# Performance work log

Hardware: AMD Instinct MI355X
Metric: run time of the kernel (lower is better)

## Reference

```python
import jax, jax.numpy as jnp
import numpy as np
import math

B = 8192
N_MODELS = 64
T_PER_SPLIT = 16
MAXLEAF = 64
EMB = 32
BN_EPS = 1e-5


def setup_inputs() -> dict:
    key = jax.random.key(0)
    k1, k2, k3 = jax.random.split(key, 3)
    # leaf indices per (sample, model*tree), values in [0, maxleaf)
    x = jax.random.randint(k1, (B, N_MODELS * T_PER_SPLIT), 0, MAXLEAF, dtype=jnp.int32)
    # embed_w ~ N(0, sqrt(1/max_ntree_per_split))
    embed_w = jax.random.normal(k2, (N_MODELS, T_PER_SPLIT * MAXLEAF, EMB), dtype=jnp.float32) * math.sqrt(1.0 / T_PER_SPLIT)
    # BatchNorm1d affine params (gamma=1, beta=0 at init)
    bn_gamma = jnp.ones((N_MODELS * EMB,), dtype=jnp.float32)
    bn_beta = jnp.zeros((N_MODELS * EMB,), dtype=jnp.float32)
    # BatchDense(n_models, embsize, 1): weight (M, E, 1) squeezed to (M, E), bias zeros (M,)
    stdv = math.sqrt(6.0 / (EMB + 1))
    bout_w = jax.random.uniform(k3, (N_MODELS, EMB), dtype=jnp.float32, minval=-stdv, maxval=stdv)
    bout_b = jnp.zeros((N_MODELS,), dtype=jnp.float32)
    return {"x": x, "embed_w": embed_w, "bn_gamma": bn_gamma, "bn_beta": bn_beta,
            "bout_w": bout_w, "bout_b": bout_b}


def reference(x, embed_w, bn_gamma, bn_beta, bout_w, bout_b):
    # x: (B, M*T) int leaf indices; embed_w: (M, T*L, E)
    Bn = x.shape[0]
    M, TL, E = embed_w.shape
    T = x.shape[1] // M
    L = TL // T
    # one_hot + bmm == per-tree gather from embed_w, summed over trees
    idx = x.reshape(Bn, M, T) + jnp.arange(T, dtype=x.dtype) * L  # (B, M, T) into TL axis
    emb = embed_w[jnp.arange(M)[None, :, None], idx]              # (B, M, T, E) gather
    h = emb.sum(axis=2).reshape(Bn, M * E)                        # (B, M*E)
    # BatchNorm1d (training-mode batch statistics, biased variance as in torch)
    mean = h.mean(axis=0)
    var = h.var(axis=0)
    h = (h - mean) / jnp.sqrt(var + BN_EPS) * bn_gamma + bn_beta
    # dropout is identity in eval mode
    h = h.reshape(Bn, M, E)
    # BatchDense: per-model linear E -> 1
    out = jnp.einsum('bme,me->bm', h, bout_w) + bout_b            # (B, M)
    sum_out = out.sum(axis=-1, keepdims=True)                     # (B, 1)
    return (sum_out, out)
```

## Files before the change

kernel.cpp:

```cpp
#include <hip/hip_runtime.h>
#include <hip/hip_fp16.h>

constexpr int B_TOT = 8192;
constexpr int NM    = 64;
constexpr int TT    = 16;
constexpr int LF    = 64;
constexpr int EM    = 32;
constexpr int XROW  = NM * TT;
constexpr int TROWS = TT * LF;

template<int TQ>
__device__ __forceinline__ int4 qbcast(int4 v) {
    constexpr int c = TQ * 0x55;
    int4 r;
    r.x = __builtin_amdgcn_mov_dpp(v.x, c, 0xf, 0xf, true);
    r.y = __builtin_amdgcn_mov_dpp(v.y, c, 0xf, 0xf, true);
    r.z = __builtin_amdgcn_mov_dpp(v.z, c, 0xf, 0xf, true);
    r.w = __builtin_amdgcn_mov_dpp(v.w, c, 0xf, 0xf, true);
    return r;
}

__device__ __forceinline__ __half2 H2(unsigned u) { return *(const __half2*)&u; }

__global__ __launch_bounds__(512, 4) void k_stats_f16(
    const int* __restrict__ x, const float* __restrict__ tbl,
    float* __restrict__ psum, float* __restrict__ psq)
{
    __shared__ uint4 tb[TROWS * 4];
    __shared__ float red[2][8][32];

    const int m     = blockIdx.x & 63;
    const int chunk = blockIdx.x >> 6;
    const int tid   = threadIdx.x;
    const int f     = tid & 3;
    const int grp   = tid >> 2;
    const int b0    = chunk * 1024;

    {
        const float4* __restrict__ src = (const float4*)(tbl + (size_t)m * (TROWS * EM));
#pragma unroll
        for (int i = 0; i < 8; ++i) {
            const int o = tid + i * 512;
            const float4 a = src[o * 2];
            const float4 c = src[o * 2 + 1];
            uint4 p;
            __half2 h0 = __floats2half2_rn(a.x, a.y);
            __half2 h1 = __floats2half2_rn(a.z, a.w);
            __half2 h2 = __floats2half2_rn(c.x, c.y);
            __half2 h3 = __floats2half2_rn(c.z, c.w);
            p.x = *(unsigned*)&h0; p.y = *(unsigned*)&h1;
            p.z = *(unsigned*)&h2; p.w = *(unsigned*)&h3;
            tb[o] = p;
        }
    }

    int4 xr = ((const int4*)(x + (size_t)(b0 + grp) * XROW + m * TT))[f];

    float s[8], s2[8];
#pragma unroll
    for (int k = 0; k < 8; ++k) { s[k] = 0.f; s2[k] = 0.f; }

    __syncthreads();

    for (int p = 0; p < 8; ++p) {
        int4 nxt;
        if (p < 7)
            nxt = ((const int4*)(x + (size_t)(b0 + (p + 1) * 128 + grp) * XROW + m * TT))[f];

        const int4 q0 = qbcast<0>(xr);
        const int4 q1 = qbcast<1>(xr);
        const int4 q2 = qbcast<2>(xr);
        const int4 q3 = qbcast<3>(xr);

        __half2 h0 = __half2(__half(0.f), __half(0.f));
        __half2 h1 = h0, h2 = h0, h3 = h0;

#define GATH(Q, RB)                                                          \
        {                                                                    \
            const uint4 a0 = tb[((Q).x + RB      ) * 4 + f];                 \
            const uint4 a1 = tb[((Q).y + RB +  64) * 4 + f];                 \
            const uint4 a2 = tb[((Q).z + RB + 128) * 4 + f];                 \
            const uint4 a3 = tb[((Q).w + RB + 192) * 4 + f];                 \
            h0 = __hadd2(h0, __hadd2(__hadd2(H2(a0.x), H2(a1.x)),            \
                                     __hadd2(H2(a2.x), H2(a3.x))));          \
            h1 = __hadd2(h1, __hadd2(__hadd2(H2(a0.y), H2(a1.y)),            \
                                     __hadd2(H2(a2.y), H2(a3.y))));          \
            h2 = __hadd2(h2, __hadd2(__hadd2(H2(a0.z), H2(a1.z)),            \
                                     __hadd2(H2(a2.z), H2(a3.z))));          \
            h3 = __hadd2(h3, __hadd2(__hadd2(H2(a0.w), H2(a1.w)),            \
                                     __hadd2(H2(a2.w), H2(a3.w))));          \
        }
        GATH(q0, 0) GATH(q1, 256) GATH(q2, 512) GATH(q3, 768)
#undef GATH

        const __half2 hv[4] = {h0, h1, h2, h3};
#pragma unroll
        for (int k = 0; k < 4; ++k) {
            const float lo = __low2float(hv[k]);
            const float hi = __high2float(hv[k]);
            s[2*k]   += lo;  s2[2*k]   = fmaf(lo, lo, s2[2*k]);
            s[2*k+1] += hi;  s2[2*k+1] = fmaf(hi, hi, s2[2*k+1]);
        }
        xr = nxt;
    }

#pragma unroll
    for (int off = 4; off <= 32; off <<= 1) {
#pragma unroll
        for (int k = 0; k < 8; ++k) {
            s[k]  += __shfl_xor(s[k],  off);
            s2[k] += __shfl_xor(s2[k], off);
        }
    }
    const int wave = tid >> 6;
    if ((tid & 63) < 4) {
#pragma unroll
        for (int k = 0; k < 8; ++k) {
            red[0][wave][f * 8 + k] = s[k];
            red[1][wave][f * 8 + k] = s2[k];
        }
    }
    __syncthreads();
    if (tid < 32) {
        float a = 0.f, a2 = 0.f;
#pragma unroll
        for (int w = 0; w < 8; ++w) { a += red[0][w][tid]; a2 += red[1][w][tid]; }
        psum[(chunk * NM + m) * EM + tid] = a;
        psq [(chunk * NM + m) * EM + tid] = a2;
    }
}

__global__ __launch_bounds__(256) void k_prep(
    const float* __restrict__ tbl,
    const float* __restrict__ gamma, const float* __restrict__ beta,
    const float* __restrict__ bw, const float* __restrict__ bb,
    const float* __restrict__ psum, const float* __restrict__ psq,
    float* __restrict__ Cm, float* __restrict__ g2)
{
    const int m    = blockIdx.x >> 2;
    const int part = blockIdx.x & 3;
    __shared__ float a_s[EM];
    if (threadIdx.x < EM) {
        const int e  = threadIdx.x;
        const int ch = m * EM + e;
        float sum = 0.f, sq = 0.f;
#pragma unroll
        for (int c = 0; c < 8; ++c) {
            sum += psum[(c * NM + m) * EM + e];
            sq  += psq [(c * NM + m) * EM + e];
        }
        const float inv_n = 1.f / (float)B_TOT;
        const float mean = sum * inv_n;
        const float var  = sq * inv_n - mean * mean;
        const float istd = rsqrtf(var + 1e-5f);
        const float g = gamma[ch];
        const float w = bw[ch];
        a_s[e] = istd * g * w;
        float ct = (beta[ch] - mean * istd * g) * w;
#pragma unroll
        for (int off = 16; off > 0; off >>= 1) ct += __shfl_down(ct, off, 32);
        if (e == 0 && part == 0) Cm[m] = bb[m] + ct;
    }
    __syncthreads();

    const float* __restrict__ tblm = tbl + (size_t)m * (TROWS * EM);
    const int row = part * 256 + threadIdx.x;
    const float4* rp = (const float4*)(tblm + row * EM);
    float acc = 0.f;
#pragma unroll
    for (int i = 0; i < 8; ++i) {
        const float4 v = rp[i];
        acc += v.x * a_s[i*4+0] + v.y * a_s[i*4+1]
             + v.z * a_s[i*4+2] + v.w * a_s[i*4+3];
    }
    g2[row * NM + m] = acc;
}

__global__ __launch_bounds__(1024, 8) void k_out(
    const int* __restrict__ x, const float* __restrict__ g2,
    const float* __restrict__ Cm, float* __restrict__ out)
{
    __shared__ float slab[4 * LF * NM];
    const int tid  = threadIdx.x;
    const int wid  = tid >> 6;
    const int lane = tid & 63;
    const int b    = blockIdx.x * 16 + wid;

    const int4* xp = (const int4*)(x + (size_t)b * XROW + lane * TT);
    const int4 q0 = xp[0], q1 = xp[1], q2 = xp[2], q3 = xp[3];
    const int idxs[16] = {q0.x,q0.y,q0.z,q0.w, q1.x,q1.y,q1.z,q1.w,
                          q2.x,q2.y,q2.z,q2.w, q3.x,q3.y,q3.z,q3.w};

    float acc = 0.f;
#pragma unroll
    for (int ph = 0; ph < 4; ++ph) {
        if (ph) __syncthreads();
        const float4* src = (const float4*)(g2 + (size_t)ph * (4 * LF * NM));
        float4* dst = (float4*)slab;
#pragma unroll
        for (int j = 0; j < 4; ++j) dst[tid + j * 1024] = src[tid + j * 1024];
        __syncthreads();
#pragma unroll
        for (int tt = 0; tt < 4; ++tt)
            acc += slab[tt * (LF * NM) + idxs[ph * 4 + tt] * NM + lane];
    }

    const float o = acc + Cm[lane];
    float s = o;
#pragma unroll
    for (int off = 32; off > 0; off >>= 1) s += __shfl_down(s, off);
    out[B_TOT + (size_t)b * NM + lane] = o;
    if (lane == 0) out[b] = s;
}

extern "C" void kernel_launch(void* const* d_in, const int* in_sizes, int n_in,
                              void* d_out, int out_size, void* d_ws, size_t ws_size,
                              hipStream_t stream) {
    const int*   x       = (const int*)d_in[0];
    const float* embed_w = (const float*)d_in[1];
    const float* gamma   = (const float*)d_in[2];
    const float* beta    = (const float*)d_in[3];
    const float* bout_w  = (const float*)d_in[4];
    const float* bout_b  = (const float*)d_in[5];
    float* out = (float*)d_out;

    float* ws   = (float*)d_ws;
    float* Cm   = ws;
    float* g2   = ws + 64;
    float* psum = ws + 64 + 65536;
    float* psq  = psum + 16384;

    k_stats_f16<<<dim3(512), dim3(512), 0, stream>>>(x, embed_w, psum, psq);
    k_prep<<<dim3(256), dim3(256),  0, stream>>>(embed_w, gamma, beta, bout_w,
                                                 bout_b, psum, psq, Cm, g2);
    k_out <<<dim3(512), dim3(1024), 0, stream>>>(x, g2, Cm, out);
}
```

Baseline: 108.0 us.

## Pack leaf indices to bytes in stats pass and process two samples per wave in output kernel

The stats kernel now writes a byte-packed copy of the leaf indices (four indices per 32-bit word) to workspace while it streams x. The output kernel reads this compact array, a quarter the size of the int32 x, instead of re-reading x. Each wave also handles two samples, so the g2 slab staged in shared memory is reused twice and only half the blocks are launched. The cost is an extra global write in the stats kernel, and the output kernel now depends on indices fitting in 8 bits.

Result: slower. 110.7 us (+2.5%).

```diff
diff --git a/kernel.cpp b/kernel.cpp
--- a/kernel.cpp
+++ b/kernel.cpp
@@ -24,7 +24,8 @@
 
 __global__ __launch_bounds__(512, 4) void k_stats_f16(
     const int* __restrict__ x, const float* __restrict__ tbl,
-    float* __restrict__ psum, float* __restrict__ psq)
+    float* __restrict__ psum, float* __restrict__ psq,
+    unsigned* __restrict__ x8)
 {
     __shared__ uint4 tb[TROWS * 4];
     __shared__ float red[2][8][32];
@@ -63,9 +64,14 @@
     __syncthreads();
 
     for (int p = 0; p < 8; ++p) {
+        const int b = b0 + p * 128 + grp;
         int4 nxt;
         if (p < 7)
-            nxt = ((const int4*)(x + (size_t)(b0 + (p + 1) * 128 + grp) * XROW + m * TT))[f];
+            nxt = ((const int4*)(x + (size_t)(b + 128) * XROW + m * TT))[f];
+
+        x8[((size_t)b * NM + m) * 4 + f] =
+            (unsigned)(xr.x & 0xff) | ((unsigned)(xr.y & 0xff) << 8) |
+            ((unsigned)(xr.z & 0xff) << 16) | ((unsigned)xr.w << 24);
 
         const int4 q0 = qbcast<0>(xr);
         const int4 q1 = qbcast<1>(xr);
@@ -176,22 +182,21 @@
     g2[row * NM + m] = acc;
 }
 
-__global__ __launch_bounds__(1024, 8) void k_out(
-    const int* __restrict__ x, const float* __restrict__ g2,
+__global__ __launch_bounds__(1024) void k_out(
+    const uint4* __restrict__ x8, const float* __restrict__ g2,
     const float* __restrict__ Cm, float* __restrict__ out)
 {
     __shared__ float slab[4 * LF * NM];
     const int tid  = threadIdx.x;
     const int wid  = tid >> 6;
     const int lane = tid & 63;
-    const int b    = blockIdx.x * 16 + wid;
-
-    const int4* xp = (const int4*)(x + (size_t)b * XROW + lane * TT);
-    const int4 q0 = xp[0], q1 = xp[1], q2 = xp[2], q3 = xp[3];
-    const int idxs[16] = {q0.x,q0.y,q0.z,q0.w, q1.x,q1.y,q1.z,q1.w,
-                          q2.x,q2.y,q2.z,q2.w, q3.x,q3.y,q3.z,q3.w};
-
-    float acc = 0.f;
+    const int bA   = blockIdx.x * 32 + wid;
+    const int bB   = bA + 16;
+
+    const uint4 pa = x8[(size_t)bA * NM + lane];
+    const uint4 pb = x8[(size_t)bB * NM + lane];
+
+    float accA = 0.f, accB = 0.f;
 #pragma unroll
     for (int ph = 0; ph < 4; ++ph) {
         if (ph) __syncthreads();
@@ -200,17 +205,30 @@
 #pragma unroll
         for (int j = 0; j < 4; ++j) dst[tid + j * 1024] = src[tid + j * 1024];
         __syncthreads();
-#pragma unroll
-        for (int tt = 0; tt < 4; ++tt)
-            acc += slab[tt * (LF * NM) + idxs[ph * 4 + tt] * NM + lane];
-    }
-
-    const float o = acc + Cm[lane];
-    float s = o;
-#pragma unroll
-    for (int off = 32; off > 0; off >>= 1) s += __shfl_down(s, off);
-    out[B_TOT + (size_t)b * NM + lane] = o;
-    if (lane == 0) out[b] = s;
+
+        const unsigned wa = (ph == 0) ? pa.x : (ph == 1) ? pa.y : (ph == 2) ? pa.z : pa.w;
+        const unsigned wb = (ph == 0) ? pb.x : (ph == 1) ? pb.y : (ph == 2) ? pb.z : pb.w;
+#pragma unroll
+        for (int k = 0; k < 4; ++k) {
+            const int ia = (wa >> (k * 8)) & 0xff;
+            const int ib = (wb >> (k * 8)) & 0xff;
+            accA += slab[k * (LF * NM) + ia * NM + lane];
+            accB += slab[k * (LF * NM) + ib * NM + lane];
+        }
+    }
+
+    const float cm = Cm[lane];
+    const float oA = accA + cm;
+    const float oB = accB + cm;
+    float sA = oA, sB = oB;
+#pragma unroll
+    for (int off = 32; off > 0; off >>= 1) {
+        sA += __shfl_down(sA, off);
+        sB += __shfl_down(sB, off);
+    }
+    out[B_TOT + (size_t)bA * NM + lane] = oA;
+    out[B_TOT + (size_t)bB * NM + lane] = oB;
+    if (lane == 0) { out[bA] = sA; out[bB] = sB; }
 }
 
 extern "C" void kernel_launch(void* const* d_in, const int* in_sizes, int n_in,
@@ -229,9 +247,10 @@
     float* g2   = ws + 64;
     float* psum = ws + 64 + 65536;
     float* psq  = psum + 16384;
-
-    k_stats_f16<<<dim3(512), dim3(512), 0, stream>>>(x, embed_w, psum, psq);
+    unsigned* x8 = (unsigned*)(psq + 16384);
+
+    k_stats_f16<<<dim3(512), dim3(512), 0, stream>>>(x, embed_w, psum, psq, x8);
     k_prep<<<dim3(256), dim3(256),  0, stream>>>(embed_w, gamma, beta, bout_w,
                                                  bout_b, psum, psq, Cm, g2);
-    k_out <<<dim3(512), dim3(1024), 0, stream>>>(x, g2, Cm, out);
-}
+    k_out <<<dim3(256), dim3(1024), 0, stream>>>((const uint4*)x8, g2, Cm, out);
+}
```
